# Kernel optimization log

Measured on AMD Instinct MI355X. Metric: run time of the kernel, lower is better.

Reference implementation:

```python
import jax, jax.numpy as jnp
import numpy as np

B, S, DM = 2, 2048, 1024
H, HD = 16, 64  # heads, head_dims = dims // heads
SCALE = HD ** -0.5


def softmax_one(x):
    # softmax with +1 in the denominator: exp(x_i) / (1 + sum_j exp(x_j))
    # stable form: shift by m = max(max(x), 0)
    m = jnp.maximum(jnp.max(x, axis=-1, keepdims=True), 0.0)
    e = jnp.exp(x - m)
    return e / (jnp.exp(-m) + jnp.sum(e, axis=-1, keepdims=True))


def setup_inputs() -> dict:
    key = jax.random.key(0)
    ks = jax.random.split(key, 11)
    init = lambda k, shape, fan_in: jax.random.uniform(k, shape, jnp.float32, -1.0, 1.0) * (fan_in ** -0.5)
    return {
        "query": jax.random.normal(ks[0], (B, S, DM), jnp.float32),
        "key": jax.random.normal(ks[1], (B, S, DM), jnp.float32),
        "value": jax.random.normal(ks[2], (B, S, DM), jnp.float32),
        "Wq": init(ks[3], (H * HD, DM), DM), "bq": init(ks[4], (H * HD,), DM),
        "Wk": init(ks[5], (H * HD, DM), DM), "bk": init(ks[6], (H * HD,), DM),
        "Wv": init(ks[7], (H * HD, DM), DM), "bv": init(ks[8], (H * HD,), DM),
        "Wo": init(ks[9], (DM, H * HD), H * HD), "bo": init(ks[10], (DM,), H * HD),
    }


def _proj(x, W, b):
    # [B,S,DM] -> [B,H,S,HD]
    y = x @ W.T + b
    return y.reshape(B, S, H, HD).transpose(0, 2, 1, 3)


def reference(query, key, value, Wq, bq, Wk, bk, Wv, bv, Wo, bo):
    Q = _proj(query, Wq, bq)
    K = _proj(key, Wk, bk)
    V = _proj(value, Wv, bv)
    scores = jnp.einsum("bhqd,bhkd->bhqk", Q, K) * SCALE  # [B,H,S,S]
    attn = softmax_one(scores)
    out = jnp.einsum("bhqk,bhkd->bhqd", attn, V)  # [B,H,S,HD]
    out = out.transpose(0, 2, 1, 3).reshape(B, S, H * HD)
    return out @ Wo.T + bo
```

## Files before the change

### kernel.cpp

```cpp
#include <hip/hip_runtime.h>

#define B_ 2
#define S_ 2048
#define DM_ 1024
#define H_ 16
#define HD_ 64
#define QSCALE_ 0.18033688011112042f

typedef __bf16 bf16;
typedef __attribute__((ext_vector_type(4))) __bf16 bf16x4;
typedef __attribute__((ext_vector_type(8))) __bf16 bf16x8;
typedef __attribute__((ext_vector_type(4))) float f32x4;

#define MFMA16(a, b, c) __builtin_amdgcn_mfma_f32_16x16x32_bf16((a), (b), (c), 0, 0, 0)
#define EXP2(x) __builtin_amdgcn_exp2f(x)

__device__ __forceinline__ void async16(const bf16* g, bf16* l) {
  __builtin_amdgcn_global_load_lds(
      (const __attribute__((address_space(1))) void*)g,
      (__attribute__((address_space(3))) void*)l, 16, 0, 0);
}

__global__ __launch_bounds__(256) void convert_kernel(
    const float* __restrict__ q, const float* __restrict__ k,
    const float* __restrict__ v, const float* __restrict__ wq,
    const float* __restrict__ wk, const float* __restrict__ wv,
    const float* __restrict__ wo, bf16* __restrict__ dst) {
  size_t idx = ((size_t)blockIdx.x * 256 + threadIdx.x) * 8;
  const float* src;
  size_t off;
  if (idx < 4194304) { src = q; off = idx; }
  else if (idx < 8388608) { src = k; off = idx - 4194304; }
  else if (idx < 12582912) { src = v; off = idx - 8388608; }
  else if (idx < 13631488) { src = wq; off = idx - 12582912; }
  else if (idx < 14680064) { src = wk; off = idx - 13631488; }
  else if (idx < 15728640) { src = wv; off = idx - 14680064; }
  else { src = wo; off = idx - 15728640; }
  float4 a = *(const float4*)(src + off);
  float4 b = *(const float4*)(src + off + 4);
  bf16x8 o;
  o[0] = (bf16)a.x; o[1] = (bf16)a.y; o[2] = (bf16)a.z; o[3] = (bf16)a.w;
  o[4] = (bf16)b.x; o[5] = (bf16)b.y; o[6] = (bf16)b.z; o[7] = (bf16)b.w;
  *(bf16x8*)(dst + idx) = o;
}

template <int MODE>
__device__ __forceinline__ void gemm_body(bf16* smem, const bf16* A,
                                          const bf16* W, const float* bias,
                                          bf16* C, float scale, int m0,
                                          int n0) {
  constexpr int K = 1024;
  bf16* As = smem;
  bf16* Bs = smem + 128 * 64;
  const int t = threadIdx.x;
  const int lane = t & 63, wave = t >> 6;
  const int quad = lane >> 4, l16 = lane & 15;
  const int wm = (wave >> 1) * 64, wn = (wave & 1) * 64;

  const f32x4 zero = {0.f, 0.f, 0.f, 0.f};
  f32x4 acc[4][4];
  for (int i = 0; i < 4; i++)
    for (int j = 0; j < 4; j++) acc[i][j] = zero;

  for (int k0 = 0; k0 < K; k0 += 64) {
    for (int i = 0; i < 4; ++i) {
      int c = i * 256 + t;
      int row = c >> 3, g = c & 7;
      int off = k0 + ((g ^ (row & 7)) * 8);
      async16(A + (size_t)(m0 + row) * K + off, As + c * 8);
      async16(W + (size_t)(n0 + row) * K + off, Bs + c * 8);
    }
    __syncthreads();

    for (int ks = 0; ks < 2; ks++) {
      bf16x8 af[4], bfr[4];
      for (int mb = 0; mb < 4; mb++) {
        int ra = wm + mb * 16 + l16;
        af[mb] = *(const bf16x8*)(As + ra * 64 + ((ks * 4 + quad) ^ (ra & 7)) * 8);
        int rb = wn + mb * 16 + l16;
        bfr[mb] = *(const bf16x8*)(Bs + rb * 64 + ((ks * 4 + quad) ^ (rb & 7)) * 8);
      }
      for (int mb = 0; mb < 4; mb++)
        for (int nb = 0; nb < 4; nb++)
          acc[mb][nb] = MFMA16(af[mb], bfr[nb], acc[mb][nb]);
    }
    __syncthreads();
  }

  if constexpr (MODE == 2) {
    bf16* Ct = smem;
    for (int nb = 0; nb < 4; nb++) {
      int cl = wn + nb * 16 + l16;
      float bv = bias[n0 + cl] * scale;
      for (int mb = 0; mb < 4; mb++) {
        int rowb = wm + mb * 16 + quad * 4;
        bf16x4 v;
        for (int r = 0; r < 4; r++)
          v[r] = (bf16)(acc[mb][nb][r] * scale + bv);
        *(bf16x4*)(Ct + cl * 136 + rowb) = v;
      }
    }
    __syncthreads();
    int c = t >> 1, half = t & 1;
    int colg = n0 + c;
    int hh = colg >> 6, dd = colg & 63;
    int bb = m0 >> 11, s0 = m0 & (S_ - 1);
    bf16* dst = C + (((size_t)(bb * H_ + hh)) * HD_ + dd) * S_ + s0 + half * 64;
    const bf16* srcr = Ct + c * 136 + half * 64;
    for (int j = 0; j < 8; ++j)
      *(bf16x8*)(dst + j * 8) = *(const bf16x8*)(srcr + j * 8);
  } else {
    for (int nb = 0; nb < 4; nb++) {
      int col = n0 + wn + nb * 16 + l16;
      float bv = bias[col] * scale;
      for (int mb = 0; mb < 4; mb++) {
        int rowb = m0 + wm + mb * 16 + quad * 4;
        for (int r = 0; r < 4; r++) {
          int row = rowb + r;
          float o = acc[mb][nb][r] * scale + bv;
          int bb = row >> 11, s = row & (S_ - 1);
          int h = col >> 6, d = col & 63;
          C[(((size_t)(bb * H_ + h)) * S_ + s) * HD_ + d] = (bf16)o;
        }
      }
    }
  }
}

__global__ __launch_bounds__(256, 4) void qkv_proj_kernel(
    const bf16* Xc, const float* bq, const float* bk, const float* bv,
    bf16* Qo, bf16* Ko, bf16* Vo) {
  __shared__ __align__(16) bf16 smem[128 * 136];
  int bid = blockIdx.x;
  int z = bid >> 8;
  int r = bid & 255;
  int c = r & 7;
  int j = r >> 3;
  int m0 = (c * 4 + (j & 3)) * 128;
  int n0 = (j >> 2) * 128;
  const bf16* A = Xc + (size_t)z * 4194304;
  const bf16* W = Xc + 12582912 + (size_t)z * 1048576;
  if (z == 0)
    gemm_body<1>(smem, A, W, bq, Qo, QSCALE_, m0, n0);
  else if (z == 1)
    gemm_body<1>(smem, A, W, bk, Ko, 1.0f, m0, n0);
  else
    gemm_body<2>(smem, A, W, bv, Vo, 1.0f, m0, n0);
}

__global__ __launch_bounds__(256, 4) void out_proj_kernel(const bf16* A,
                                                          const bf16* W,
                                                          const float* bias,
                                                          float* C) {
  constexpr int K = 1024, N = 1024;
  __shared__ __align__(16) bf16 As[64 * 64];
  __shared__ __align__(16) bf16 Bs[64 * 64];
  const int t = threadIdx.x;
  const int lane = t & 63, wave = t >> 6;
  const int quad = lane >> 4, l16 = lane & 15;
  int bid = blockIdx.x;
  int c = bid & 7;
  int j = bid >> 3;
  const int m0 = (c * 8 + (j & 7)) * 64;
  const int n0 = (j >> 3) * 64;

  const f32x4 zero = {0.f, 0.f, 0.f, 0.f};
  f32x4 acc[4];
  for (int i = 0; i < 4; i++) acc[i] = zero;

  for (int k0 = 0; k0 < K; k0 += 64) {
    for (int i = 0; i < 2; ++i) {
      int cc = i * 256 + t;
      int row = cc >> 3, g = cc & 7;
      int off = k0 + ((g ^ (row & 7)) * 8);
      async16(A + (size_t)(m0 + row) * K + off, As + cc * 8);
      async16(W + (size_t)(n0 + row) * K + off, Bs + cc * 8);
    }
    __syncthreads();

    for (int ks = 0; ks < 2; ks++) {
      int ra = wave * 16 + l16;
      bf16x8 af = *(const bf16x8*)(As + ra * 64 + ((ks * 4 + quad) ^ (ra & 7)) * 8);
      for (int nb = 0; nb < 4; nb++) {
        int rb = nb * 16 + l16;
        bf16x8 bfr =
            *(const bf16x8*)(Bs + rb * 64 + ((ks * 4 + quad) ^ (rb & 7)) * 8);
        acc[nb] = MFMA16(af, bfr, acc[nb]);
      }
    }
    __syncthreads();
  }

  for (int nb = 0; nb < 4; nb++) {
    int col = n0 + nb * 16 + l16;
    float bv = bias[col];
    int rowb = m0 + wave * 16 + quad * 4;
    for (int r = 0; r < 4; r++)
      C[(size_t)(rowb + r) * N + col] = acc[nb][r] + bv;
  }
}

__global__ __launch_bounds__(256, 2) void attn_kernel(
    const bf16* __restrict__ Q, const bf16* __restrict__ Kg,
    const bf16* __restrict__ VTg, bf16* __restrict__ O) {
  __shared__ __align__(16) bf16 Ks[128 * 64];
  __shared__ __align__(16) bf16 Vt[64 * 128];
  __shared__ __align__(16) bf16 Ps[4 * 64 * 72];
  __shared__ float rsL[2][64];
  const int t = threadIdx.x;
  const int lane = t & 63, wave = t >> 6;
  const int quad = lane >> 4, l16 = lane & 15;
  const int id = blockIdx.x;
  const int bh = id & 31;
  const int qt = id >> 5;
  const int q0 = qt * 128;
  const int b = bh >> 4, h = bh & 15;
  const int qhalf = wave >> 1, khalf = wave & 1;
  const size_t base = ((size_t)(b * H_ + h)) * S_ * HD_;
  const bf16* Qp = Q + base;
  const bf16* Kp = Kg + base;
  const bf16* Vp = VTg + base;

  bf16x8 aq[4][2];
  for (int s = 0; s < 4; s++) {
    const bf16* qr = Qp + (size_t)(q0 + qhalf * 64 + s * 16 + l16) * HD_;
    aq[s][0] = *(const bf16x8*)(qr + quad * 8);
    aq[s][1] = *(const bf16x8*)(qr + 32 + quad * 8);
  }

  const f32x4 zero = {0.f, 0.f, 0.f, 0.f};
  f32x4 oc[4][4];
  for (int s = 0; s < 4; s++)
    for (int d = 0; d < 4; d++) oc[s][d] = zero;
  float rs[4] = {0.f, 0.f, 0.f, 0.f};

  bf16* Pw = Ps + wave * (64 * 72);

  for (int kv0 = 0; kv0 < S_; kv0 += 128) {
    for (int i = 0; i < 4; ++i) {
      int c = i * 256 + t;
      int row = c >> 3, g = c & 7;
      async16(Kp + (size_t)(kv0 + row) * HD_ + (g ^ (row & 7)) * 8, Ks + c * 8);
    }
    for (int i = 0; i < 4; ++i) {
      int c = i * 256 + t;
      int d = c >> 4, g = c & 15;
      async16(Vp + (size_t)d * S_ + kv0 + (g ^ (d & 15)) * 8, Vt + c * 8);
    }
    __syncthreads();

    f32x4 sc[4][4];
    for (int s = 0; s < 4; s++)
      for (int nb = 0; nb < 4; nb++) sc[s][nb] = zero;
    for (int ks = 0; ks < 2; ks++) {
      for (int nb = 0; nb < 4; nb++) {
        int row = khalf * 64 + nb * 16 + l16;
        int slot = (ks * 4 + quad) ^ (row & 7);
        bf16x8 kf = *(const bf16x8*)(Ks + row * 64 + slot * 8);
        for (int s = 0; s < 4; s++)
          sc[s][nb] = MFMA16(kf, aq[s][ks], sc[s][nb]);
      }
    }

    for (int s = 0; s < 4; s++) {
      bf16* prow = Pw + (s * 16 + l16) * 72 + quad * 4;
      for (int nb = 0; nb < 4; nb++) {
        float p0 = EXP2(sc[s][nb][0]);
        float p1 = EXP2(sc[s][nb][1]);
        float p2 = EXP2(sc[s][nb][2]);
        float p3 = EXP2(sc[s][nb][3]);
        rs[s] += (p0 + p1) + (p2 + p3);
        bf16x4 pv = {(bf16)p0, (bf16)p1, (bf16)p2, (bf16)p3};
        *(bf16x4*)(prow + nb * 16) = pv;
      }
    }

    for (int ks2 = 0; ks2 < 2; ks2++) {
      bf16x8 vf[4];
      for (int db = 0; db < 4; db++) {
        int row = db * 16 + l16;
        int g = khalf * 8 + ks2 * 4 + quad;
        vf[db] = *(const bf16x8*)(Vt + row * 128 + (g ^ (row & 15)) * 8);
      }
      for (int s = 0; s < 4; s++) {
        bf16x8 ap =
            *(const bf16x8*)(Pw + (s * 16 + l16) * 72 + ks2 * 32 + quad * 8);
        for (int db = 0; db < 4; db++)
          oc[s][db] = MFMA16(ap, vf[db], oc[s][db]);
      }
    }
    __syncthreads();
  }

  float* Ld = (float*)Ps;
  if (khalf) {
    for (int s = 0; s < 4; s++) {
      float rtot = rs[s];
      rtot += __shfl_xor(rtot, 16);
      rtot += __shfl_xor(rtot, 32);
      if (quad == 0) rsL[qhalf][s * 16 + l16] = rtot;
      for (int db = 0; db < 4; db++)
        for (int r = 0; r < 4; r++)
          Ld[(size_t)qhalf * (64 * 68) + (s * 16 + quad * 4 + r) * 68 +
             db * 16 + l16] = oc[s][db][r];
    }
  }
  __syncthreads();
  if (!khalf) {
    for (int s = 0; s < 4; s++) {
      float rtot = rs[s];
      rtot += __shfl_xor(rtot, 16);
      rtot += __shfl_xor(rtot, 32);
      float l_all = 1.f + rtot + rsL[qhalf][s * 16 + l16];
      for (int r = 0; r < 4; r++) {
        float inv = 1.f / __shfl(l_all, quad * 4 + r);
        int qrow = q0 + qhalf * 64 + s * 16 + quad * 4 + r;
        size_t orow = ((size_t)(b * S_ + qrow) * H_ + h) * HD_;
        for (int db = 0; db < 4; db++) {
          float val = oc[s][db][r] +
                      Ld[(size_t)qhalf * (64 * 68) +
                         (s * 16 + quad * 4 + r) * 68 + db * 16 + l16];
          O[orow + db * 16 + l16] = (bf16)(val * inv);
        }
      }
    }
  }
}

extern "C" void kernel_launch(void* const* d_in, const int* in_sizes, int n_in,
                              void* d_out, int out_size, void* d_ws,
                              size_t ws_size, hipStream_t stream) {
  const float* query = (const float*)d_in[0];
  const float* key = (const float*)d_in[1];
  const float* value = (const float*)d_in[2];
  const float* bq = (const float*)d_in[4];
  const float* bk = (const float*)d_in[6];
  const float* bv = (const float*)d_in[8];
  const float* bo = (const float*)d_in[10];
  float* out = (float*)d_out;

  bf16* Xc = (bf16*)d_ws;
  bf16* Qw = Xc + 16777216;
  const size_t SZ = (size_t)B_ * H_ * S_ * HD_;
  bf16* Kw = Qw + SZ;
  bf16* Vw = Kw + SZ;
  bf16* Ow = Vw + SZ;

  convert_kernel<<<8192, 256, 0, stream>>>(query, key, value,
                                           (const float*)d_in[3],
                                           (const float*)d_in[5],
                                           (const float*)d_in[7],
                                           (const float*)d_in[9], Xc);
  qkv_proj_kernel<<<768, 256, 0, stream>>>(Xc, bq, bk, bv, Qw, Kw, Vw);
  attn_kernel<<<512, 256, 0, stream>>>(Qw, Kw, Vw, Ow);
  out_proj_kernel<<<1024, 256, 0, stream>>>(Ow, Xc + 15728640, bo, out);
}
```

Measured before the change: 206.1 us.

## Prefetch next KV tile through registers in attention and enlarge out-proj M tile

```diff
diff --git a/kernel.cpp b/kernel.cpp
--- a/kernel.cpp
+++ b/kernel.cpp
@@ -153,7 +153,7 @@
                                                           const float* bias,
                                                           float* C) {
   constexpr int K = 1024, N = 1024;
-  __shared__ __align__(16) bf16 As[64 * 64];
+  __shared__ __align__(16) bf16 As[128 * 64];
   __shared__ __align__(16) bf16 Bs[64 * 64];
   const int t = threadIdx.x;
   const int lane = t & 63, wave = t >> 6;
@@ -161,32 +161,44 @@
   int bid = blockIdx.x;
   int c = bid & 7;
   int j = bid >> 3;
-  const int m0 = (c * 8 + (j & 7)) * 64;
-  const int n0 = (j >> 3) * 64;
+  const int m0 = (c * 4 + (j & 3)) * 128;
+  const int n0 = (j >> 2) * 64;
+  const int wm = wave * 32;
 
   const f32x4 zero = {0.f, 0.f, 0.f, 0.f};
-  f32x4 acc[4];
-  for (int i = 0; i < 4; i++) acc[i] = zero;
+  f32x4 acc[2][4];
+  for (int i = 0; i < 2; i++)
+    for (int jn = 0; jn < 4; jn++) acc[i][jn] = zero;
 
   for (int k0 = 0; k0 < K; k0 += 64) {
+    for (int i = 0; i < 4; ++i) {
+      int cc = i * 256 + t;
+      int row = cc >> 3, g = cc & 7;
+      int off = k0 + ((g ^ (row & 7)) * 8);
+      async16(A + (size_t)(m0 + row) * K + off, As + cc * 8);
+    }
     for (int i = 0; i < 2; ++i) {
       int cc = i * 256 + t;
       int row = cc >> 3, g = cc & 7;
       int off = k0 + ((g ^ (row & 7)) * 8);
-      async16(A + (size_t)(m0 + row) * K + off, As + cc * 8);
       async16(W + (size_t)(n0 + row) * K + off, Bs + cc * 8);
     }
     __syncthreads();
 
     for (int ks = 0; ks < 2; ks++) {
-      int ra = wave * 16 + l16;
-      bf16x8 af = *(const bf16x8*)(As + ra * 64 + ((ks * 4 + quad) ^ (ra & 7)) * 8);
+      bf16x8 af[2], bfr[4];
+      for (int mb = 0; mb < 2; mb++) {
+        int ra = wm + mb * 16 + l16;
+        af[mb] = *(const bf16x8*)(As + ra * 64 + ((ks * 4 + quad) ^ (ra & 7)) * 8);
+      }
       for (int nb = 0; nb < 4; nb++) {
         int rb = nb * 16 + l16;
-        bf16x8 bfr =
+        bfr[nb] =
             *(const bf16x8*)(Bs + rb * 64 + ((ks * 4 + quad) ^ (rb & 7)) * 8);
-        acc[nb] = MFMA16(af, bfr, acc[nb]);
-      }
+      }
+      for (int mb = 0; mb < 2; mb++)
+        for (int nb = 0; nb < 4; nb++)
+          acc[mb][nb] = MFMA16(af[mb], bfr[nb], acc[mb][nb]);
     }
     __syncthreads();
   }
@@ -194,9 +206,11 @@
   for (int nb = 0; nb < 4; nb++) {
     int col = n0 + nb * 16 + l16;
     float bv = bias[col];
-    int rowb = m0 + wave * 16 + quad * 4;
-    for (int r = 0; r < 4; r++)
-      C[(size_t)(rowb + r) * N + col] = acc[nb][r] + bv;
+    for (int mb = 0; mb < 2; mb++) {
+      int rowb = m0 + wm + mb * 16 + quad * 4;
+      for (int r = 0; r < 4; r++)
+        C[(size_t)(rowb + r) * N + col] = acc[mb][nb][r] + bv;
+    }
   }
 }
 
@@ -236,18 +250,35 @@
 
   bf16* Pw = Ps + wave * (64 * 72);
 
+  for (int i = 0; i < 4; ++i) {
+    int cc = i * 256 + t;
+    int row = cc >> 3, g = cc & 7;
+    async16(Kp + (size_t)row * HD_ + (g ^ (row & 7)) * 8, Ks + cc * 8);
+  }
+  for (int i = 0; i < 4; ++i) {
+    int cc = i * 256 + t;
+    int d = cc >> 4, g = cc & 15;
+    async16(Vp + (size_t)d * S_ + (g ^ (d & 15)) * 8, Vt + cc * 8);
+  }
+  __syncthreads();
+
   for (int kv0 = 0; kv0 < S_; kv0 += 128) {
-    for (int i = 0; i < 4; ++i) {
-      int c = i * 256 + t;
-      int row = c >> 3, g = c & 7;
-      async16(Kp + (size_t)(kv0 + row) * HD_ + (g ^ (row & 7)) * 8, Ks + c * 8);
-    }
-    for (int i = 0; i < 4; ++i) {
-      int c = i * 256 + t;
-      int d = c >> 4, g = c & 15;
-      async16(Vp + (size_t)d * S_ + kv0 + (g ^ (d & 15)) * 8, Vt + c * 8);
-    }
-    __syncthreads();
+    const bool pf = (kv0 + 128) < S_;
+    float4 kr[4], vr[4];
+    if (pf) {
+      const int kv1 = kv0 + 128;
+      for (int i = 0; i < 4; ++i) {
+        int cc = i * 256 + t;
+        int row = cc >> 3, g = cc & 7;
+        kr[i] = *(const float4*)(Kp + (size_t)(kv1 + row) * HD_ +
+                                 (g ^ (row & 7)) * 8);
+      }
+      for (int i = 0; i < 4; ++i) {
+        int cc = i * 256 + t;
+        int d = cc >> 4, g = cc & 15;
+        vr[i] = *(const float4*)(Vp + (size_t)d * S_ + kv1 + (g ^ (d & 15)) * 8);
+      }
+    }
 
     f32x4 sc[4][4];
     for (int s = 0; s < 4; s++)
@@ -257,8 +288,10 @@
         int row = khalf * 64 + nb * 16 + l16;
         int slot = (ks * 4 + quad) ^ (row & 7);
         bf16x8 kf = *(const bf16x8*)(Ks + row * 64 + slot * 8);
+        __builtin_amdgcn_s_setprio(1);
         for (int s = 0; s < 4; s++)
           sc[s][nb] = MFMA16(kf, aq[s][ks], sc[s][nb]);
+        __builtin_amdgcn_s_setprio(0);
       }
     }
 
@@ -285,8 +318,19 @@
       for (int s = 0; s < 4; s++) {
         bf16x8 ap =
             *(const bf16x8*)(Pw + (s * 16 + l16) * 72 + ks2 * 32 + quad * 8);
+        __builtin_amdgcn_s_setprio(1);
         for (int db = 0; db < 4; db++)
           oc[s][db] = MFMA16(ap, vf[db], oc[s][db]);
+        __builtin_amdgcn_s_setprio(0);
+      }
+    }
+
+    __syncthreads();
+    if (pf) {
+      for (int i = 0; i < 4; ++i) {
+        int cc = i * 256 + t;
+        *(float4*)(Ks + cc * 8) = kr[i];
+        *(float4*)(Vt + cc * 8) = vr[i];
       }
     }
     __syncthreads();
@@ -353,5 +397,5 @@
                                            (const float*)d_in[9], Xc);
   qkv_proj_kernel<<<768, 256, 0, stream>>>(Xc, bq, bk, bv, Qw, Kw, Vw);
   attn_kernel<<<512, 256, 0, stream>>>(Qw, Kw, Vw, Ow);
-  out_proj_kernel<<<1024, 256, 0, stream>>>(Ow, Xc + 15728640, bo, out);
-}
+  out_proj_kernel<<<512, 256, 0, stream>>>(Ow, Xc + 15728640, bo, out);
+}
```

New measurement: 255.2 us. +23.8%, slower.

## Prefetch next K/V tile into registers during compute, add MFMA priority

Applied to the files above, without the earlier changes.

```diff
diff --git a/kernel.cpp b/kernel.cpp
--- a/kernel.cpp
+++ b/kernel.cpp
@@ -236,18 +236,30 @@
 
   bf16* Pw = Ps + wave * (64 * 72);
 
+  const int krow = t >> 3, kg = t & 7;
+  const int vd = t >> 4, vg = t & 15;
+  const bf16* kbase = Kp + (size_t)krow * HD_ + (kg ^ (krow & 7)) * 8;
+  const bf16* vbase = Vp + (size_t)vd * S_ + (vg ^ (vd & 15)) * 8;
+
+  for (int i = 0; i < 4; ++i) {
+    int cc = i * 256 + t;
+    int row = cc >> 3, g = cc & 7;
+    async16(Kp + (size_t)row * HD_ + (g ^ (row & 7)) * 8, Ks + cc * 8);
+  }
+  for (int i = 0; i < 4; ++i) {
+    int cc = i * 256 + t;
+    int d = cc >> 4, g = cc & 15;
+    async16(Vp + (size_t)d * S_ + (g ^ (d & 15)) * 8, Vt + cc * 8);
+  }
+  __syncthreads();
+
   for (int kv0 = 0; kv0 < S_; kv0 += 128) {
-    for (int i = 0; i < 4; ++i) {
-      int c = i * 256 + t;
-      int row = c >> 3, g = c & 7;
-      async16(Kp + (size_t)(kv0 + row) * HD_ + (g ^ (row & 7)) * 8, Ks + c * 8);
-    }
-    for (int i = 0; i < 4; ++i) {
-      int c = i * 256 + t;
-      int d = c >> 4, g = c & 15;
-      async16(Vp + (size_t)d * S_ + kv0 + (g ^ (d & 15)) * 8, Vt + c * 8);
-    }
-    __syncthreads();
+    const int kv1 = (kv0 + 128) & (S_ - 1);
+
+    float4 kr0 = *(const float4*)(kbase + (size_t)(kv1) * HD_);
+    float4 kr1 = *(const float4*)(kbase + (size_t)(kv1 + 32) * HD_);
+    float4 kr2 = *(const float4*)(kbase + (size_t)(kv1 + 64) * HD_);
+    float4 kr3 = *(const float4*)(kbase + (size_t)(kv1 + 96) * HD_);
 
     f32x4 sc[4][4];
     for (int s = 0; s < 4; s++)
@@ -257,10 +269,17 @@
         int row = khalf * 64 + nb * 16 + l16;
         int slot = (ks * 4 + quad) ^ (row & 7);
         bf16x8 kf = *(const bf16x8*)(Ks + row * 64 + slot * 8);
+        __builtin_amdgcn_s_setprio(1);
         for (int s = 0; s < 4; s++)
           sc[s][nb] = MFMA16(kf, aq[s][ks], sc[s][nb]);
-      }
-    }
+        __builtin_amdgcn_s_setprio(0);
+      }
+    }
+
+    float4 vr0 = *(const float4*)(vbase + kv1);
+    float4 vr1 = *(const float4*)(vbase + 16 * S_ + kv1);
+    float4 vr2 = *(const float4*)(vbase + 32 * S_ + kv1);
+    float4 vr3 = *(const float4*)(vbase + 48 * S_ + kv1);
 
     for (int s = 0; s < 4; s++) {
       bf16* prow = Pw + (s * 16 + l16) * 72 + quad * 4;
@@ -285,10 +304,22 @@
       for (int s = 0; s < 4; s++) {
         bf16x8 ap =
             *(const bf16x8*)(Pw + (s * 16 + l16) * 72 + ks2 * 32 + quad * 8);
+        __builtin_amdgcn_s_setprio(1);
         for (int db = 0; db < 4; db++)
           oc[s][db] = MFMA16(ap, vf[db], oc[s][db]);
-      }
-    }
+        __builtin_amdgcn_s_setprio(0);
+      }
+    }
+
+    __syncthreads();
+    *(float4*)(Ks + (size_t)t * 8) = kr0;
+    *(float4*)(Ks + (size_t)(256 + t) * 8) = kr1;
+    *(float4*)(Ks + (size_t)(512 + t) * 8) = kr2;
+    *(float4*)(Ks + (size_t)(768 + t) * 8) = kr3;
+    *(float4*)(Vt + (size_t)t * 8) = vr0;
+    *(float4*)(Vt + (size_t)(256 + t) * 8) = vr1;
+    *(float4*)(Vt + (size_t)(512 + t) * 8) = vr2;
+    *(float4*)(Vt + (size_t)(768 + t) * 8) = vr3;
     __syncthreads();
   }
 
```

Result: slower. 210.4 us (+2.1%).

## Double-buffer K/V tiles in attention and split P staging into halves

Applied to the files above, without the earlier changes.

```diff
diff --git a/kernel.cpp b/kernel.cpp
--- a/kernel.cpp
+++ b/kernel.cpp
@@ -200,13 +200,25 @@
   }
 }
 
+__device__ __forceinline__ void stage_tile(const bf16* Kp, const bf16* Vp,
+                                           int kv, bf16* Ksb, bf16* Vtb,
+                                           int t) {
+  for (int i = 0; i < 4; ++i) {
+    int cc = i * 256 + t;
+    int row = cc >> 3, g = cc & 7;
+    async16(Kp + (size_t)(kv + row) * HD_ + (g ^ (row & 7)) * 8, Ksb + cc * 8);
+  }
+  for (int i = 0; i < 4; ++i) {
+    int cc = i * 256 + t;
+    int d = cc >> 4, g = cc & 15;
+    async16(Vp + (size_t)d * S_ + kv + (g ^ (d & 15)) * 8, Vtb + cc * 8);
+  }
+}
+
 __global__ __launch_bounds__(256, 2) void attn_kernel(
     const bf16* __restrict__ Q, const bf16* __restrict__ Kg,
     const bf16* __restrict__ VTg, bf16* __restrict__ O) {
-  __shared__ __align__(16) bf16 Ks[128 * 64];
-  __shared__ __align__(16) bf16 Vt[64 * 128];
-  __shared__ __align__(16) bf16 Ps[4 * 64 * 72];
-  __shared__ float rsL[2][64];
+  __shared__ __align__(16) bf16 smem[40960];
   const int t = threadIdx.x;
   const int lane = t & 63, wave = t >> 6;
   const int quad = lane >> 4, l16 = lane & 15;
@@ -234,20 +246,18 @@
     for (int d = 0; d < 4; d++) oc[s][d] = zero;
   float rs[4] = {0.f, 0.f, 0.f, 0.f};
 
-  bf16* Pw = Ps + wave * (64 * 72);
+  bf16* Pw = smem + 32768 + wave * (64 * 32);
+
+  stage_tile(Kp, Vp, 0, smem, smem + 8192, t);
+  __syncthreads();
 
   for (int kv0 = 0; kv0 < S_; kv0 += 128) {
-    for (int i = 0; i < 4; ++i) {
-      int c = i * 256 + t;
-      int row = c >> 3, g = c & 7;
-      async16(Kp + (size_t)(kv0 + row) * HD_ + (g ^ (row & 7)) * 8, Ks + c * 8);
-    }
-    for (int i = 0; i < 4; ++i) {
-      int c = i * 256 + t;
-      int d = c >> 4, g = c & 15;
-      async16(Vp + (size_t)d * S_ + kv0 + (g ^ (d & 15)) * 8, Vt + c * 8);
-    }
-    __syncthreads();
+    const int cur = (kv0 >> 7) & 1;
+    bf16* Ksc = smem + cur * 16384;
+    bf16* Vtc = Ksc + 8192;
+    bf16* Ksn = smem + (cur ^ 1) * 16384;
+    bf16* Vtn = Ksn + 8192;
+    stage_tile(Kp, Vp, (kv0 + 128) & (S_ - 1), Ksn, Vtn, t);
 
     f32x4 sc[4][4];
     for (int s = 0; s < 4; s++)
@@ -256,49 +266,50 @@
       for (int nb = 0; nb < 4; nb++) {
         int row = khalf * 64 + nb * 16 + l16;
         int slot = (ks * 4 + quad) ^ (row & 7);
-        bf16x8 kf = *(const bf16x8*)(Ks + row * 64 + slot * 8);
+        bf16x8 kf = *(const bf16x8*)(Ksc + row * 64 + slot * 8);
         for (int s = 0; s < 4; s++)
           sc[s][nb] = MFMA16(kf, aq[s][ks], sc[s][nb]);
       }
     }
 
-    for (int s = 0; s < 4; s++) {
-      bf16* prow = Pw + (s * 16 + l16) * 72 + quad * 4;
-      for (int nb = 0; nb < 4; nb++) {
-        float p0 = EXP2(sc[s][nb][0]);
-        float p1 = EXP2(sc[s][nb][1]);
-        float p2 = EXP2(sc[s][nb][2]);
-        float p3 = EXP2(sc[s][nb][3]);
-        rs[s] += (p0 + p1) + (p2 + p3);
-        bf16x4 pv = {(bf16)p0, (bf16)p1, (bf16)p2, (bf16)p3};
-        *(bf16x4*)(prow + nb * 16) = pv;
-      }
-    }
-
-    for (int ks2 = 0; ks2 < 2; ks2++) {
+    for (int seg = 0; seg < 2; seg++) {
+      for (int s = 0; s < 4; s++) {
+        bf16* prow = Pw + (s * 16 + l16) * 32 + quad * 4;
+        for (int nbl = 0; nbl < 2; nbl++) {
+          int nb = seg * 2 + nbl;
+          float p0 = EXP2(sc[s][nb][0]);
+          float p1 = EXP2(sc[s][nb][1]);
+          float p2 = EXP2(sc[s][nb][2]);
+          float p3 = EXP2(sc[s][nb][3]);
+          rs[s] += (p0 + p1) + (p2 + p3);
+          bf16x4 pv = {(bf16)p0, (bf16)p1, (bf16)p2, (bf16)p3};
+          *(bf16x4*)(prow + nbl * 16) = pv;
+        }
+      }
       bf16x8 vf[4];
       for (int db = 0; db < 4; db++) {
         int row = db * 16 + l16;
-        int g = khalf * 8 + ks2 * 4 + quad;
-        vf[db] = *(const bf16x8*)(Vt + row * 128 + (g ^ (row & 15)) * 8);
+        int g = khalf * 8 + seg * 4 + quad;
+        vf[db] = *(const bf16x8*)(Vtc + row * 128 + (g ^ (row & 15)) * 8);
       }
       for (int s = 0; s < 4; s++) {
-        bf16x8 ap =
-            *(const bf16x8*)(Pw + (s * 16 + l16) * 72 + ks2 * 32 + quad * 8);
+        bf16x8 ap = *(const bf16x8*)(Pw + (s * 16 + l16) * 32 + quad * 8);
         for (int db = 0; db < 4; db++)
           oc[s][db] = MFMA16(ap, vf[db], oc[s][db]);
       }
     }
-    __syncthreads();
-  }
-
-  float* Ld = (float*)Ps;
+
+    __syncthreads();
+  }
+
+  float* Ld = (float*)smem;
+  float* rsL = (float*)(smem + 17408);
   if (khalf) {
     for (int s = 0; s < 4; s++) {
       float rtot = rs[s];
       rtot += __shfl_xor(rtot, 16);
       rtot += __shfl_xor(rtot, 32);
-      if (quad == 0) rsL[qhalf][s * 16 + l16] = rtot;
+      if (quad == 0) rsL[qhalf * 64 + s * 16 + l16] = rtot;
       for (int db = 0; db < 4; db++)
         for (int r = 0; r < 4; r++)
           Ld[(size_t)qhalf * (64 * 68) + (s * 16 + quad * 4 + r) * 68 +
@@ -311,7 +322,7 @@
       float rtot = rs[s];
       rtot += __shfl_xor(rtot, 16);
       rtot += __shfl_xor(rtot, 32);
-      float l_all = 1.f + rtot + rsL[qhalf][s * 16 + l16];
+      float l_all = 1.f + rtot + rsL[qhalf * 64 + s * 16 + l16];
       for (int r = 0; r < 4; r++) {
         float inv = 1.f / __shfl(l_all, quad * 4 + r);
         int qrow = q0 + qhalf * 64 + s * 16 + quad * 4 + r;
```

After: 224.6 us. 9.0% more time.
